# Kernel optimization log

Hardware: AMD Instinct MI355X
Metric: run time of the kernel (lower is better)

The kernel has to match this reference:

```python
import jax, jax.numpy as jnp
import numpy as np

B, T, H, NUM_LAYERS = 8, 4096, 1024, 2


def _log_g(x):
    # log of g(x) = where(x>=0, x+0.5, sigmoid(x)), computed stably in log space
    return jnp.where(x >= 0.0, jnp.log(jax.nn.relu(x) + 0.5), -jax.nn.softplus(-x))


def _heinsen_scan(log_coeffs, log_values):
    # parallel scan for h_t = a_t * h_{t-1} + b_t in log space, along time axis 1
    a_star = jnp.cumsum(log_coeffs, axis=1)                       # [B,T,H]
    return jnp.exp(a_star + jax.lax.cumlogsumexp(log_values - a_star, axis=1))


def setup_inputs() -> dict:
    key = jax.random.key(0)
    k0, k1, k2 = jax.random.split(key, 3)
    scale = 1.0 / np.sqrt(H)
    return {
        "h": jax.random.normal(k0, (B, T, H), dtype=jnp.float32),
        "W0": jax.random.normal(k1, (H, 3 * H), dtype=jnp.float32) * scale,
        "W1": jax.random.normal(k2, (H, 3 * H), dtype=jnp.float32) * scale,
    }


def reference(h, W0, W1):
    for W in (W0, W1):
        z = jnp.einsum('bth,hk->btk', h, W)                       # [B,T,3H]
        hidden, gate, proj = jnp.split(z, 3, axis=-1)             # each [B,T,H]
        log_coeffs = -jax.nn.softplus(gate)                       # log(1 - sigmoid(gate))
        log_values = -jax.nn.softplus(-gate) + _log_g(hidden)     # log(sigmoid(gate)*g(hidden))
        out = _heinsen_scan(log_coeffs, log_values)               # [B,T,H]
        g = jax.nn.sigmoid(proj)
        h = g * out + (1.0 - g) * h                               # highway gate
    return h
```

## Files before the change

kernel.cpp:

```cpp
#include <hip/hip_runtime.h>

#define Bc 8
#define Td 4096
#define Hd 1024
#define N3 3072
#define Md (Bc*Td)
#define Kd Hd

#define NC 64
#define CL (Td/NC)

#define BM2 256
#define BN2 256
#define BK2 64
#define NT (Kd/BK2)

typedef _Float16 half8 __attribute__((ext_vector_type(8)));
typedef _Float16 half4v __attribute__((ext_vector_type(4)));
typedef float floatx4 __attribute__((ext_vector_type(4)));

typedef __attribute__((address_space(3))) unsigned int lds_u32;
typedef __attribute__((address_space(1))) const unsigned int glob_u32;

__device__ __forceinline__ void async_lds16(const void* g, void* l) {
    __builtin_amdgcn_global_load_lds((glob_u32*)g, (lds_u32*)l, 16, 0, 0);
}

__device__ __forceinline__ float sigm(float x) {
    return 1.0f / (1.0f + __expf(-x));
}
__device__ __forceinline__ float gfun(float x) {
    float e = __expf(-fabsf(x));
    return (x >= 0.0f) ? (x + 0.5f) : e / (1.0f + e);
}

__global__ void cvt16(const float4* __restrict__ x, half4v* __restrict__ y, int n4) {
    int i = blockIdx.x * blockDim.x + threadIdx.x;
    if (i < n4) {
        float4 v = x[i];
        half4v o;
        o[0] = (_Float16)v.x; o[1] = (_Float16)v.y;
        o[2] = (_Float16)v.z; o[3] = (_Float16)v.w;
        y[i] = o;
    }
}

__global__ void wtrans(const float* __restrict__ W, _Float16* __restrict__ Wt) {
    __shared__ float t[32][33];
    int n0 = blockIdx.x * 32, k0 = blockIdx.y * 32;
    int tx = threadIdx.x, ty = threadIdx.y;
    t[ty][tx] = W[(size_t)(k0 + ty) * N3 + n0 + tx];
    __syncthreads();
    Wt[(size_t)(n0 + ty) * Kd + k0 + tx] = (_Float16)t[tx][ty];
}

__global__ __launch_bounds__(512, 2) void gemm_f16_bt_256(
    const _Float16* __restrict__ A,
    const _Float16* __restrict__ Bt,
    _Float16* __restrict__ C)
{
    __shared__ _Float16 As[2][BM2 * BK2];
    __shared__ _Float16 Bs[2][BN2 * BK2];

    const int tid  = threadIdx.x;
    const int wave = tid >> 6;
    const int lane = tid & 63;

    const int bid = blockIdx.x;
    const int swz = (bid & 7) * (1536 / 8) + (bid >> 3);
    const int by  = swz / 12;
    const int bx  = swz - by * 12;
    const int bm  = by * BM2;
    const int bn  = bx * BN2;

    const int wm   = (wave >> 2) * 128;
    const int wn   = (wave & 3) * 64;
    const int quad = lane >> 4;
    const int lr   = lane & 15;

    floatx4 acc[8][4];
#pragma unroll
    for (int i = 0; i < 8; ++i)
#pragma unroll
        for (int j = 0; j < 4; ++j) { floatx4 z = {0.f,0.f,0.f,0.f}; acc[i][j] = z; }

    auto stageA = [&](int sel, int kt) {
        const int k0 = kt * BK2;
#pragma unroll
        for (int r = 0; r < 4; ++r) {
            int m  = r * 64 + wave * 8 + (lane >> 3);
            int kc = ((lane & 7) ^ (m & 7)) << 3;
            const _Float16* ga = A + (size_t)(bm + m) * Kd + (k0 + kc);
            char* la = (char*)&As[sel][0] + (r * 64 + wave * 8) * 128;
            async_lds16(ga, la);
        }
    };
    auto stageB = [&](int sel, int kt) {
        const int k0 = kt * BK2;
#pragma unroll
        for (int r = 0; r < 4; ++r) {
            int m  = r * 64 + wave * 8 + (lane >> 3);
            int kc = ((lane & 7) ^ (m & 7)) << 3;
            const _Float16* gb = Bt + (size_t)(bn + m) * Kd + (k0 + kc);
            char* lb = (char*)&Bs[sel][0] + (r * 64 + wave * 8) * 128;
            async_lds16(gb, lb);
        }
    };

    auto dsA = [&](int sel, int ihalf, half8 (&af)[4][2]) {
#pragma unroll
        for (int i = 0; i < 4; ++i) {
            int row = wm + (ihalf * 4 + i) * 16 + lr;
#pragma unroll
            for (int ks = 0; ks < 2; ++ks) {
                int ck = ((ks * 4 + quad) ^ (row & 7)) << 3;
                af[i][ks] = *(const half8*)&As[sel][row * BK2 + ck];
            }
        }
    };
    auto dsB = [&](int sel, int jhalf, half8 (&bf)[2][2]) {
#pragma unroll
        for (int j = 0; j < 2; ++j) {
            int row = wn + (jhalf * 2 + j) * 16 + lr;
#pragma unroll
            for (int ks = 0; ks < 2; ++ks) {
                int ck = ((ks * 4 + quad) ^ (row & 7)) << 3;
                bf[j][ks] = *(const half8*)&Bs[sel][row * BK2 + ck];
            }
        }
    };
    auto mmac = [&](int ihalf, int jhalf, half8 (&af)[4][2], half8 (&bf)[2][2]) {
        __builtin_amdgcn_s_setprio(1);
#pragma unroll
        for (int i = 0; i < 4; ++i)
#pragma unroll
            for (int j = 0; j < 2; ++j)
#pragma unroll
                for (int ks = 0; ks < 2; ++ks)
                    acc[ihalf * 4 + i][jhalf * 2 + j] =
                        __builtin_amdgcn_mfma_f32_16x16x32_f16(
                            af[i][ks], bf[j][ks],
                            acc[ihalf * 4 + i][jhalf * 2 + j], 0, 0, 0);
        __builtin_amdgcn_s_setprio(0);
    };

    auto compute_tile = [&](int sel) {
        half8 af[4][2];
        half8 bflo[2][2], bfhi[2][2];
        dsA(sel, 0, af); dsB(sel, 0, bflo);
        __builtin_amdgcn_s_barrier();
        mmac(0, 0, af, bflo);
        __builtin_amdgcn_s_barrier();
        dsB(sel, 1, bfhi);
        __builtin_amdgcn_s_barrier();
        mmac(0, 1, af, bfhi);
        __builtin_amdgcn_s_barrier();
        dsA(sel, 1, af);
        __builtin_amdgcn_s_barrier();
        mmac(1, 0, af, bflo);
        __builtin_amdgcn_s_barrier();
        mmac(1, 1, af, bfhi);
    };

    stageA(0, 0); stageB(0, 0);
    stageA(1, 1); stageB(1, 1);
    asm volatile("s_waitcnt vmcnt(8)" ::: "memory");
    __builtin_amdgcn_s_barrier();

    for (int t = 0; t < NT - 2; ++t) {
        const int sel = t & 1;
        compute_tile(sel);
        stageA(sel, t + 2); stageB(sel, t + 2);
        asm volatile("s_waitcnt vmcnt(8)" ::: "memory");
        __builtin_amdgcn_s_barrier();
    }
    compute_tile(0);
    asm volatile("s_waitcnt vmcnt(0)" ::: "memory");
    __builtin_amdgcn_s_barrier();
    compute_tile(1);

#pragma unroll
    for (int i = 0; i < 8; ++i) {
#pragma unroll
        for (int j = 0; j < 4; ++j) {
            int row0 = bm + wm + i * 16 + quad * 4;
            int col  = bn + wn + j * 16 + lr;
#pragma unroll
            for (int r = 0; r < 4; ++r)
                C[(size_t)(row0 + r) * N3 + col] = (_Float16)acc[i][j][r];
        }
    }
}

__global__ __launch_bounds__(256) void scan_phase1(
    const _Float16* __restrict__ Z, float* __restrict__ cA, float* __restrict__ cB)
{
    int ch = threadIdx.x * 4;
    int c  = blockIdx.y;
    int b  = blockIdx.z;
    const _Float16* zp = Z + ((size_t)(b * Td + c * CL)) * N3 + ch;
    float Ap[4] = {1.f, 1.f, 1.f, 1.f};
    float Bv[4] = {0.f, 0.f, 0.f, 0.f};
#pragma unroll 4
    for (int t = 0; t < CL; ++t) {
        half4v h4 = *(const half4v*)(zp);
        half4v g4 = *(const half4v*)(zp + Hd);
#pragma unroll
        for (int i = 0; i < 4; ++i) {
            float sg = sigm((float)g4[i]);
            float at = 1.0f - sg;
            float bt = sg * gfun((float)h4[i]);
            Ap[i] *= at;
            Bv[i] = fmaf(at, Bv[i], bt);
        }
        zp += N3;
    }
    size_t o = ((size_t)b * NC + c) * Hd + ch;
    *(float4*)&cA[o] = make_float4(Ap[0], Ap[1], Ap[2], Ap[3]);
    *(float4*)&cB[o] = make_float4(Bv[0], Bv[1], Bv[2], Bv[3]);
}

__global__ void scan_phase2(const float* __restrict__ cA, const float* __restrict__ cB,
                            float* __restrict__ cS)
{
    int u = (blockIdx.x * 256 + threadIdx.x) * 4;
    int b = u >> 10, ch = u & 1023;
    float4 s = make_float4(0.f, 0.f, 0.f, 0.f);
    for (int c = 0; c < NC; ++c) {
        size_t o = ((size_t)b * NC + c) * Hd + ch;
        *(float4*)&cS[o] = s;
        float4 a = *(const float4*)&cA[o];
        float4 v = *(const float4*)&cB[o];
        s.x = fmaf(a.x, s.x, v.x);
        s.y = fmaf(a.y, s.y, v.y);
        s.z = fmaf(a.z, s.z, v.z);
        s.w = fmaf(a.w, s.w, v.w);
    }
}

__global__ __launch_bounds__(256) void scan_phase3(
    const _Float16* __restrict__ Z, const float* __restrict__ cS,
    const float* __restrict__ hin32, const _Float16* __restrict__ hin16,
    float* __restrict__ hout32, _Float16* __restrict__ hout16)
{
    int ch = threadIdx.x * 4;
    int c  = blockIdx.y;
    int b  = blockIdx.z;
    float s[4];
    {
        float4 s4 = *(const float4*)&cS[((size_t)b * NC + c) * Hd + ch];
        s[0] = s4.x; s[1] = s4.y; s[2] = s4.z; s[3] = s4.w;
    }
    const _Float16* zp = Z + ((size_t)(b * Td + c * CL)) * N3 + ch;
    size_t ho = ((size_t)(b * Td + c * CL)) * Hd + ch;
#pragma unroll 2
    for (int t = 0; t < CL; ++t) {
        half4v h4 = *(const half4v*)(zp);
        half4v g4 = *(const half4v*)(zp + Hd);
        half4v p4 = *(const half4v*)(zp + 2 * Hd);
        float hi[4];
        if (hin32) {
            float4 v = *(const float4*)&hin32[ho];
            hi[0] = v.x; hi[1] = v.y; hi[2] = v.z; hi[3] = v.w;
        } else {
            half4v v = *(const half4v*)&hin16[ho];
#pragma unroll
            for (int i = 0; i < 4; ++i) hi[i] = (float)v[i];
        }
        float o[4];
#pragma unroll
        for (int i = 0; i < 4; ++i) {
            float sg = sigm((float)g4[i]);
            float at = 1.0f - sg;
            s[i] = fmaf(at, s[i], sg * gfun((float)h4[i]));
            float gg = sigm((float)p4[i]);
            o[i] = fmaf(gg, s[i] - hi[i], hi[i]);
        }
        if (hout32) *(float4*)&hout32[ho] = make_float4(o[0], o[1], o[2], o[3]);
        if (hout16) {
            half4v v;
#pragma unroll
            for (int i = 0; i < 4; ++i) v[i] = (_Float16)o[i];
            *(half4v*)&hout16[ho] = v;
        }
        zp += N3; ho += Hd;
    }
}

extern "C" void kernel_launch(void* const* d_in, const int* in_sizes, int n_in,
                              void* d_out, int out_size, void* d_ws, size_t ws_size,
                              hipStream_t stream) {
    const float* h  = (const float*)d_in[0];
    const float* W0 = (const float*)d_in[1];
    const float* W1 = (const float*)d_in[2];
    float* out = (float*)d_out;

    char* ws = (char*)d_ws;
    _Float16* Z    = (_Float16*)ws; ws += (size_t)Md * N3 * 2;
    _Float16* Hbf  = (_Float16*)ws; ws += (size_t)Md * Kd * 2;
    _Float16* Wt   = (_Float16*)ws; ws += (size_t)N3 * Kd * 2;
    float* cA   = (float*)ws; ws += (size_t)Bc * NC * Hd * 4;
    float* cB   = (float*)ws; ws += (size_t)Bc * NC * Hd * 4;
    float* cS   = (float*)ws; ws += (size_t)Bc * NC * Hd * 4;

    {
        int n4 = Md * Kd / 4;
        cvt16<<<n4 / 256, 256, 0, stream>>>((const float4*)h, (half4v*)Hbf, n4);
    }

    for (int l = 0; l < 2; ++l) {
        const float* W = l ? W1 : W0;

        wtrans<<<dim3(N3 / 32, Kd / 32), dim3(32, 32), 0, stream>>>(W, Wt);
        gemm_f16_bt_256<<<dim3((Md / BM2) * (N3 / BN2)), 512, 0, stream>>>(Hbf, Wt, Z);
        scan_phase1<<<dim3(1, NC, Bc), 256, 0, stream>>>(Z, cA, cB);
        scan_phase2<<<(Bc * Hd / 4) / 256, 256, 0, stream>>>(cA, cB, cS);
        if (l == 0) {
            scan_phase3<<<dim3(1, NC, Bc), 256, 0, stream>>>(
                Z, cS, h, nullptr, nullptr, Hbf);
        } else {
            scan_phase3<<<dim3(1, NC, Bc), 256, 0, stream>>>(
                Z, cS, nullptr, Hbf, out, nullptr);
        }
    }
}
```

Measured before the change: 1.078 ms.

## Stream GEMM loads in half-tile segments and double scan chunk count

The GEMM mainloop now issues global-to-LDS loads as quarter-tile segments (half of A or half of B) interleaved between MFMA sub-blocks. This keeps memory traffic in flight continuously instead of loading whole tiles between compute phases, with wait counts and barriers placed around each segment. The scan uses 128 chunks instead of 64, giving the chunked scan phases more parallelism at the cost of a longer serial phase 2. Phase 2 also writes its carry-in prefix over cB in place, removing the separate cS buffer.

```diff
diff --git a/kernel.cpp b/kernel.cpp
--- a/kernel.cpp
+++ b/kernel.cpp
@@ -7,13 +7,14 @@
 #define Md (Bc*Td)
 #define Kd Hd
 
-#define NC 64
+#define NC 128
 #define CL (Td/NC)
 
 #define BM2 256
 #define BN2 256
 #define BK2 64
 #define NT (Kd/BK2)
+#define NSEG (4*NT)
 
 typedef _Float16 half8 __attribute__((ext_vector_type(8)));
 typedef _Float16 half4v __attribute__((ext_vector_type(4)));
@@ -59,8 +60,7 @@
     const _Float16* __restrict__ Bt,
     _Float16* __restrict__ C)
 {
-    __shared__ _Float16 As[2][BM2 * BK2];
-    __shared__ _Float16 Bs[2][BN2 * BK2];
+    __shared__ _Float16 lds[2][4][128 * 64];
 
     const int tid  = threadIdx.x;
     const int wave = tid >> 6;
@@ -77,6 +77,9 @@
     const int wn   = (wave & 3) * 64;
     const int quad = lane >> 4;
     const int lr   = lane & 15;
+    const int aslot = wm ? 3 : 0;
+    const int bslot = (wn >= 128) ? 2 : 1;
+    const int bro   = wn & 127;
 
     floatx4 acc[8][4];
 #pragma unroll
@@ -84,52 +87,50 @@
 #pragma unroll
         for (int j = 0; j < 4; ++j) { floatx4 z = {0.f,0.f,0.f,0.f}; acc[i][j] = z; }
 
-    auto stageA = [&](int sel, int kt) {
-        const int k0 = kt * BK2;
-#pragma unroll
-        for (int r = 0; r < 4; ++r) {
-            int m  = r * 64 + wave * 8 + (lane >> 3);
-            int kc = ((lane & 7) ^ (m & 7)) << 3;
-            const _Float16* ga = A + (size_t)(bm + m) * Kd + (k0 + kc);
-            char* la = (char*)&As[sel][0] + (r * 64 + wave * 8) * 128;
-            async_lds16(ga, la);
+    auto stage_seg = [&](int seg) {
+        const int tt    = seg >> 2;
+        const int b     = seg & 3;
+        const int sel   = tt & 1;
+        const int k0    = tt * BK2;
+        const bool isA  = (b & 1);
+        const int rbase = (b >= 2) ? 128 : 0;
+        const int slot  = (b < 2) ? (1 - b) : b;
+        const _Float16* src = isA ? A : Bt;
+        const int g0    = (isA ? bm : bn) + rbase;
+#pragma unroll
+        for (int r = 0; r < 2; ++r) {
+            int rl = r * 64 + wave * 8 + (lane >> 3);
+            int kc = ((lane & 7) ^ (rl & 7)) << 3;
+            const _Float16* g = src + (size_t)(g0 + rl) * Kd + (k0 + kc);
+            char* l = (char*)&lds[sel][slot][0] + (r * 64 + wave * 8) * 128;
+            async_lds16(g, l);
         }
     };
-    auto stageB = [&](int sel, int kt) {
-        const int k0 = kt * BK2;
-#pragma unroll
-        for (int r = 0; r < 4; ++r) {
-            int m  = r * 64 + wave * 8 + (lane >> 3);
-            int kc = ((lane & 7) ^ (m & 7)) << 3;
-            const _Float16* gb = Bt + (size_t)(bn + m) * Kd + (k0 + kc);
-            char* lb = (char*)&Bs[sel][0] + (r * 64 + wave * 8) * 128;
-            async_lds16(gb, lb);
-        }
-    };
-
-    auto dsA = [&](int sel, int ihalf, half8 (&af)[4][2]) {
+
+    auto dsA = [&](int sel, int ih, half8 (&af)[4][2]) {
 #pragma unroll
         for (int i = 0; i < 4; ++i) {
-            int row = wm + (ihalf * 4 + i) * 16 + lr;
+            int row = (ih * 4 + i) * 16 + lr;
 #pragma unroll
             for (int ks = 0; ks < 2; ++ks) {
                 int ck = ((ks * 4 + quad) ^ (row & 7)) << 3;
-                af[i][ks] = *(const half8*)&As[sel][row * BK2 + ck];
+                af[i][ks] = *(const half8*)&lds[sel][aslot][row * 64 + ck];
             }
         }
     };
-    auto dsB = [&](int sel, int jhalf, half8 (&bf)[2][2]) {
+    auto dsB = [&](int sel, int jh, half8 (&bf)[2][2]) {
 #pragma unroll
         for (int j = 0; j < 2; ++j) {
-            int row = wn + (jhalf * 2 + j) * 16 + lr;
+            int row = bro + (jh * 2 + j) * 16 + lr;
 #pragma unroll
             for (int ks = 0; ks < 2; ++ks) {
                 int ck = ((ks * 4 + quad) ^ (row & 7)) << 3;
-                bf[j][ks] = *(const half8*)&Bs[sel][row * BK2 + ck];
+                bf[j][ks] = *(const half8*)&lds[sel][bslot][row * 64 + ck];
             }
         }
     };
-    auto mmac = [&](int ihalf, int jhalf, half8 (&af)[4][2], half8 (&bf)[2][2]) {
+    auto mmac = [&](int ih, int jh, half8 (&af)[4][2], half8 (&bf)[2][2]) {
+        __builtin_amdgcn_sched_barrier(0);
         __builtin_amdgcn_s_setprio(1);
 #pragma unroll
         for (int i = 0; i < 4; ++i)
@@ -137,47 +138,51 @@
             for (int j = 0; j < 2; ++j)
 #pragma unroll
                 for (int ks = 0; ks < 2; ++ks)
-                    acc[ihalf * 4 + i][jhalf * 2 + j] =
+                    acc[ih * 4 + i][jh * 2 + j] =
                         __builtin_amdgcn_mfma_f32_16x16x32_f16(
                             af[i][ks], bf[j][ks],
-                            acc[ihalf * 4 + i][jhalf * 2 + j], 0, 0, 0);
+                            acc[ih * 4 + i][jh * 2 + j], 0, 0, 0);
         __builtin_amdgcn_s_setprio(0);
+        __builtin_amdgcn_sched_barrier(0);
     };
 
-    auto compute_tile = [&](int sel) {
-        half8 af[4][2];
-        half8 bflo[2][2], bfhi[2][2];
-        dsA(sel, 0, af); dsB(sel, 0, bflo);
-        __builtin_amdgcn_s_barrier();
-        mmac(0, 0, af, bflo);
-        __builtin_amdgcn_s_barrier();
-        dsB(sel, 1, bfhi);
-        __builtin_amdgcn_s_barrier();
-        mmac(0, 1, af, bfhi);
-        __builtin_amdgcn_s_barrier();
+    half8 af[4][2], bf0[2][2], bf1[2][2];
+
+    for (int s = 0; s < 6; ++s) stage_seg(s);
+    asm volatile("s_waitcnt vmcnt(4)" ::: "memory");
+    asm volatile("s_barrier" ::: "memory");
+
+    for (int kt = 0; kt < NT; ++kt) {
+        const int sel = kt & 1;
+        const int p = kt * 4;
+        dsA(sel, 0, af); dsB(sel, 0, bf0);
+        if (p + 6 < NSEG) stage_seg(p + 6);
+        asm volatile("s_barrier" ::: "memory");
+        mmac(0, 0, af, bf0);
+        asm volatile("s_waitcnt lgkmcnt(0)" ::: "memory");
+        asm volatile("s_barrier" ::: "memory");
+        dsB(sel, 1, bf1);
+        if (p + 7 < NSEG) stage_seg(p + 7);
+        asm volatile("s_barrier" ::: "memory");
+        mmac(0, 1, af, bf1);
+        asm volatile("s_waitcnt lgkmcnt(0)" ::: "memory");
+        asm volatile("s_barrier" ::: "memory");
         dsA(sel, 1, af);
-        __builtin_amdgcn_s_barrier();
-        mmac(1, 0, af, bflo);
-        __builtin_amdgcn_s_barrier();
-        mmac(1, 1, af, bfhi);
-    };
-
-    stageA(0, 0); stageB(0, 0);
-    stageA(1, 1); stageB(1, 1);
-    asm volatile("s_waitcnt vmcnt(8)" ::: "memory");
-    __builtin_amdgcn_s_barrier();
-
-    for (int t = 0; t < NT - 2; ++t) {
-        const int sel = t & 1;
-        compute_tile(sel);
-        stageA(sel, t + 2); stageB(sel, t + 2);
-        asm volatile("s_waitcnt vmcnt(8)" ::: "memory");
-        __builtin_amdgcn_s_barrier();
-    }
-    compute_tile(0);
-    asm volatile("s_waitcnt vmcnt(0)" ::: "memory");
-    __builtin_amdgcn_s_barrier();
-    compute_tile(1);
+        if (p + 8 < NSEG) stage_seg(p + 8);
+        asm volatile("s_barrier" ::: "memory");
+        mmac(1, 0, af, bf0);
+        asm volatile("s_waitcnt lgkmcnt(0)" ::: "memory");
+        asm volatile("s_barrier" ::: "memory");
+        if (p + 9 < NSEG) stage_seg(p + 9);
+        mmac(1, 1, af, bf1);
+        if (kt < NT - 2) {
+            asm volatile("s_waitcnt vmcnt(4)" ::: "memory");
+            asm volatile("s_barrier" ::: "memory");
+        } else if (kt == NT - 2) {
+            asm volatile("s_waitcnt vmcnt(0)" ::: "memory");
+            asm volatile("s_barrier" ::: "memory");
+        }
+    }
 
 #pragma unroll
     for (int i = 0; i < 8; ++i) {
@@ -220,17 +225,16 @@
     *(float4*)&cB[o] = make_float4(Bv[0], Bv[1], Bv[2], Bv[3]);
 }
 
-__global__ void scan_phase2(const float* __restrict__ cA, const float* __restrict__ cB,
-                            float* __restrict__ cS)
+__global__ void scan_phase2(const float* __restrict__ cA, float* __restrict__ cB)
 {
     int u = (blockIdx.x * 256 + threadIdx.x) * 4;
     int b = u >> 10, ch = u & 1023;
     float4 s = make_float4(0.f, 0.f, 0.f, 0.f);
     for (int c = 0; c < NC; ++c) {
         size_t o = ((size_t)b * NC + c) * Hd + ch;
-        *(float4*)&cS[o] = s;
         float4 a = *(const float4*)&cA[o];
         float4 v = *(const float4*)&cB[o];
+        *(float4*)&cB[o] = s;
         s.x = fmaf(a.x, s.x, v.x);
         s.y = fmaf(a.y, s.y, v.y);
         s.z = fmaf(a.z, s.z, v.z);
@@ -301,7 +305,6 @@
     _Float16* Wt   = (_Float16*)ws; ws += (size_t)N3 * Kd * 2;
     float* cA   = (float*)ws; ws += (size_t)Bc * NC * Hd * 4;
     float* cB   = (float*)ws; ws += (size_t)Bc * NC * Hd * 4;
-    float* cS   = (float*)ws; ws += (size_t)Bc * NC * Hd * 4;
 
     {
         int n4 = Md * Kd / 4;
@@ -314,13 +317,13 @@
         wtrans<<<dim3(N3 / 32, Kd / 32), dim3(32, 32), 0, stream>>>(W, Wt);
         gemm_f16_bt_256<<<dim3((Md / BM2) * (N3 / BN2)), 512, 0, stream>>>(Hbf, Wt, Z);
         scan_phase1<<<dim3(1, NC, Bc), 256, 0, stream>>>(Z, cA, cB);
-        scan_phase2<<<(Bc * Hd / 4) / 256, 256, 0, stream>>>(cA, cB, cS);
+        scan_phase2<<<(Bc * Hd / 4) / 256, 256, 0, stream>>>(cA, cB);
         if (l == 0) {
             scan_phase3<<<dim3(1, NC, Bc), 256, 0, stream>>>(
-                Z, cS, h, nullptr, nullptr, Hbf);
+                Z, cB, h, nullptr, nullptr, Hbf);
         } else {
             scan_phase3<<<dim3(1, NC, Bc), 256, 0, stream>>>(
-                Z, cS, nullptr, Hbf, out, nullptr);
-        }
-    }
-}
+                Z, cB, nullptr, Hbf, out, nullptr);
+        }
+    }
+}
```

Measured after the change: 922.3 us. 1.17x faster.
